# Performance work log

Hardware: AMD Instinct MI355X
Metric: run time of the kernel (lower is better)

## Reference

```python
import jax, jax.numpy as jnp
import numpy as np

B, C, H, W = 8, 256, 128, 128
NH, WS = 8, 8
HD = C // NH
WNH, WNW = H // WS, W // WS


def _rel_pos_index():
    coords = np.stack(np.meshgrid(np.arange(WS), np.arange(WS), indexing='ij'))  # [2,ws,ws]
    flat = coords.reshape(2, -1)
    rel = (flat[:, :, None] - flat[:, None, :]).transpose(1, 2, 0)  # [ws^2,ws^2,2]
    rel[..., 0] += WS - 1
    rel[..., 1] += WS - 1
    rel[..., 0] *= 2 * WS - 1
    return jnp.asarray(rel.sum(-1))  # [ws^2,ws^2]


def grid_sample(img, grid):
    # Bilinear, padding_mode='zeros', align_corners=True. img [N,C,H,W], grid [N,Hg,Wg,2] (x,y in [-1,1])
    N, Ci, Hi, Wi = img.shape
    gx = (grid[..., 0] + 1.0) * 0.5 * (Wi - 1)
    gy = (grid[..., 1] + 1.0) * 0.5 * (Hi - 1)
    x0 = jnp.floor(gx)
    y0 = jnp.floor(gy)
    x0i = x0.astype(jnp.int32)
    y0i = y0.astype(jnp.int32)
    wx1 = gx - x0
    wx0 = 1.0 - wx1
    wy1 = gy - y0
    wy0 = 1.0 - wy1
    nb = jnp.arange(N)[:, None, None]

    def corner(yi, xi, wgt):
        valid = (yi >= 0) & (yi < Hi) & (xi >= 0) & (xi < Wi)
        yc = jnp.clip(yi, 0, Hi - 1)
        xc = jnp.clip(xi, 0, Wi - 1)
        val = img[nb, :, yc, xc]  # [N,Hg,Wg,C]
        return val * (wgt * valid)[..., None]

    out = (corner(y0i, x0i, wy0 * wx0) + corner(y0i, x0i + 1, wy0 * wx1)
           + corner(y0i + 1, x0i, wy1 * wx0) + corner(y0i + 1, x0i + 1, wy1 * wx1))
    return jnp.transpose(out, (0, 3, 1, 2))


def setup_inputs() -> dict:
    key = jax.random.key(0)
    ks = jax.random.split(key, 10)
    f = lambda k, s, sc=1.0: jax.random.normal(k, s, dtype=jnp.float32) * sc
    return {
        'x': f(ks[0], (B, C, H, W)),
        'qkv_w': f(ks[1], (3 * C, C), 0.02),
        'qkv_b': f(ks[2], (3 * C,), 0.02),
        'bias_w': f(ks[3], (2 * NH, C), 0.02),
        'bias_b': f(ks[4], (2 * NH,), 0.02),
        'scale_w': f(ks[5], (2 * NH, C), 0.02),
        'scale_b': f(ks[6], (2 * NH,), 0.02),
        'proj_w': f(ks[7], (C, C), 0.02),
        'proj_b': f(ks[8], (C,), 0.02),
        'rpb_table': f(ks[9], ((2 * WS - 1) ** 2, NH), 0.02),
    }


def reference(x, qkv_w, qkv_b, bias_w, bias_b, scale_w, scale_b, proj_w, proj_b, rpb_table):
    scale = HD ** -0.5
    N = B * NH
    # ---- deterministic base sampling coordinates (shift=0, no padding since H,W % WS == 0) ----
    lin_w = jnp.linspace(-1.0, 1.0, W)
    lin_h = jnp.linspace(-1.0, 1.0, H)
    winref_w = lin_w.reshape(WNW, WS).mean(-1)  # window centers along width
    winref_h = lin_h.reshape(WNH, WS).mean(-1)
    off_w = jnp.arange(WS) * 2.0 / (W - 1)
    off_w = off_w - off_w.mean()
    off_h = jnp.arange(WS) * 2.0 / (H - 1)
    off_h = off_h - off_h.mean()
    base_x = jnp.broadcast_to(winref_w[None, None, :, None] + off_w[None, None, None, :], (WNH, WS, WNW, WS))
    base_y = jnp.broadcast_to((winref_h[:, None] + off_h[None, :])[:, :, None, None], (WNH, WS, WNW, WS))
    # ---- predicted per-head per-window biases & scales ----
    xp = jax.nn.leaky_relu(x.reshape(B, C, WNH, WS, WNW, WS).mean((3, 5)))  # [B,C,WNH,WNW]
    biases = (jnp.einsum('oc,bchw->bohw', bias_w, xp) + bias_b[None, :, None, None]).reshape(N, 2, WNH, WNW)
    bx = biases[:, 0] / WNW  # sampling_biases[:,0] / (w // ws)
    by = biases[:, 1] / WNH
    scales = (jnp.einsum('oc,bchw->bohw', scale_w, xp) + scale_b[None, :, None, None]).reshape(N, 2, WNH, WNW)
    sx, sy = scales[:, 0], scales[:, 1]
    # final = base + local_offsets * scale + bias (broadcast [N,WNH,1,WNW,1] over window interior)
    cx = base_x[None] + off_w[None, None, None, None, :] * sx[:, :, None, :, None] + bx[:, :, None, :, None]
    cy = base_y[None] + off_h[None, None, :, None, None] * sy[:, :, None, :, None] + by[:, :, None, :, None]
    grid = jnp.stack([cx, cy], -1).reshape(N, H, W, 2)
    # ---- qkv via 1x1 conv ----
    qkv = (jnp.einsum('oc,bchw->bohw', qkv_w, x) + qkv_b[None, :, None, None]).reshape(B, 3, NH, HD, H, W)
    q = qkv[:, 0].reshape(N, HD, H, W)
    k = qkv[:, 1].reshape(N, HD, H, W)
    v = qkv[:, 2].reshape(N, HD, H, W)
    ksamp = grid_sample(k, grid)
    vsamp = grid_sample(v, grid)

    def win(t):  # [N,HD,H,W] -> [B, nWin, NH, WS*WS, HD]
        t = t.reshape(B, NH, HD, WNH, WS, WNW, WS)
        return jnp.transpose(t, (0, 3, 5, 1, 4, 6, 2)).reshape(B, WNH * WNW, NH, WS * WS, HD)

    qw, kw, vw = win(q), win(ksamp), win(vsamp)
    rpb = jnp.transpose(rpb_table[_rel_pos_index().reshape(-1)].reshape(WS * WS, WS * WS, NH), (2, 0, 1))
    attn = jnp.einsum('bwhqd,bwhkd->bwhqk', qw, kw) * scale + rpb[None, None]
    attn = jax.nn.softmax(attn, axis=-1)
    out = jnp.einsum('bwhqk,bwhkd->bwhqd', attn, vw)
    out = out.reshape(B, WNH, WNW, NH, WS, WS, HD)
    out = jnp.transpose(out, (0, 3, 6, 1, 4, 2, 5)).reshape(B, C, H, W)
    out = jnp.einsum('oc,bchw->bohw', proj_w, out) + proj_b[None, :, None, None]
    return out
```

## Files before the change

kernel.cpp:

```cpp
#include <hip/hip_runtime.h>
#include <hip/hip_fp16.h>

#define B_ 8
#define C_ 256
#define H_ 128
#define W_ 128
#define NH_ 8
#define WS_ 8
#define HD_ 32
#define WN_ 16
#define NWIN_ 256
#define HW_ 16384

typedef unsigned short ushort_t;
typedef unsigned int uint_t;
typedef __attribute__((ext_vector_type(8))) short short8;
typedef _Float16 __attribute__((ext_vector_type(8))) half8;
typedef __attribute__((ext_vector_type(4))) float f32x4;

__device__ __forceinline__ ushort_t bf16_rtn(float x) {
    uint_t u = __float_as_uint(x);
    return (ushort_t)((u + 0x7FFFu + ((u >> 16) & 1u)) >> 16);
}
__device__ __forceinline__ uint_t bfpack(float a, float b) {
    return (uint_t)bf16_rtn(a) | ((uint_t)bf16_rtn(b) << 16);
}
__device__ __forceinline__ uint_t h2pack(float a, float b) {
    __half2 h = __floats2half2_rn(a, b);
    return __builtin_bit_cast(uint_t, h);
}
__device__ __forceinline__ void gload_lds16(const void* g, void* l) {
    __builtin_amdgcn_global_load_lds(
        (const __attribute__((address_space(1))) unsigned int*)g,
        (__attribute__((address_space(3))) unsigned int*)l,
        16, 0, 0);
}

__global__ __launch_bounds__(256) void wpack_kernel(const float* __restrict__ w,
                            ushort_t* __restrict__ wpk) {
    int u = blockIdx.x*256 + threadIdx.x;
    int lane = u & 63;
    int f    = (u >> 6) & 3;
    int kk   = (u >> 8) & 1;
    int ks   = (u >> 9) & 3;
    int wm   = (u >> 11) & 1;
    int oc   = u >> 12;
    int o = oc*128 + wm*64 + f*16 + (lane & 15);
    int c = ks*64 + kk*32 + (lane >> 4)*8;
    const float* src = w + (size_t)o*256 + c;
    float4 v0 = *(const float4*)src;
    float4 v1 = *(const float4*)(src + 4);
    uint4 Hv;
    Hv.x = bfpack(v0.x, v0.y); Hv.y = bfpack(v0.z, v0.w);
    Hv.z = bfpack(v1.x, v1.y); Hv.w = bfpack(v1.z, v1.w);
    ((uint4*)wpk)[u] = Hv;
}

__global__ __launch_bounds__(256) void wconv_kernel(const float* __restrict__ w,
                            ushort_t* __restrict__ wh, int n4) {
    int i = blockIdx.x*256 + threadIdx.x;
    if (i >= n4) return;
    float4 v = ((const float4*)w)[i];
    ((uint2*)wh)[i] = make_uint2(bfpack(v.x, v.y), bfpack(v.z, v.w));
}

__global__ __launch_bounds__(256) void rpb_expand_kernel(const float* __restrict__ rpb_table,
                            float* __restrict__ rpbT) {
    int nh = blockIdx.x;
    int t = threadIdx.x;
    #pragma unroll
    for (int rr = 0; rr < 16; ++rr) {
        int e = t*16 + rr;
        int kcol = e >> 6, qrow = e & 63;
        int yq = qrow >> 3, xq = qrow & 7, yk = kcol >> 3, xk = kcol & 7;
        int idx = (yq - yk + 7)*15 + (xq - xk + 7);
        rpbT[((size_t)nh*64 + kcol)*64 + qrow] = rpb_table[idx*8 + nh];
    }
}

__global__ __launch_bounds__(256) void transpose_split_kernel(const float* __restrict__ x,
                            ushort_t* __restrict__ th, float* __restrict__ xpart) {
    __shared__ float tile[64][65];
    int b = blockIdx.z;
    int p0 = blockIdx.x * 64, c0 = blockIdx.y * 64;
    const float* xsrc = x + (size_t)b*C_*HW_;
    int t = threadIdx.x;
    #pragma unroll
    for (int r = 0; r < 4; ++r) {
        int task = t + r*256;
        int cl = task >> 4, p4 = (task & 15) * 4;
        float4 v = *(const float4*)(xsrc + (size_t)(c0+cl)*HW_ + p0 + p4);
        tile[cl][p4+0] = v.x; tile[cl][p4+1] = v.y; tile[cl][p4+2] = v.z; tile[cl][p4+3] = v.w;
    }
    __syncthreads();
    {
        int h = blockIdx.x >> 1, wbase = (blockIdx.x & 1) * 8;
        #pragma unroll
        for (int r = 0; r < 2; ++r) {
            int task = t + r*256;
            int cl = task >> 3, wx = task & 7;
            float s = 0.f;
            #pragma unroll
            for (int j = 0; j < 8; ++j) s += tile[cl][wx*8+j];
            xpart[(((size_t)b*256 + c0+cl)*128 + h)*16 + wbase + wx] = s;
        }
    }
    ushort_t* thb = th + (size_t)b*HW_*256;
    #pragma unroll
    for (int r = 0; r < 2; ++r) {
        int task = t + r*256;
        int pl = task >> 3, cb = (task & 7) * 8;
        uint4 Hh;
        Hh.x = bfpack(tile[cb+0][pl], tile[cb+1][pl]);
        Hh.y = bfpack(tile[cb+2][pl], tile[cb+3][pl]);
        Hh.z = bfpack(tile[cb+4][pl], tile[cb+5][pl]);
        Hh.w = bfpack(tile[cb+6][pl], tile[cb+7][pl]);
        *(uint4*)(thb + (size_t)(p0+pl)*256 + c0 + cb) = Hh;
    }
}

__global__ __launch_bounds__(256) void pool2_kernel(const float* __restrict__ xpart, float* __restrict__ xp) {
    int bc = blockIdx.x;
    int t = threadIdx.x;
    int wy = t >> 4, wxg = t & 15;
    const float* src = xpart + (size_t)bc*2048;
    float s = 0.f;
    #pragma unroll
    for (int i = 0; i < 8; ++i) s += src[(wy*8+i)*16 + wxg];
    s *= (1.f/64.f);
    xp[(size_t)bc*256 + t] = s > 0.f ? s : 0.01f*s;
}

__global__ __launch_bounds__(256) void params_kernel(const float* __restrict__ xp,
                              const float* __restrict__ bias_w, const float* __restrict__ bias_b,
                              const float* __restrict__ scale_w, const float* __restrict__ scale_b,
                              float* __restrict__ params) {
    __shared__ float xs[256];
    int blk = blockIdx.x;
    int b = blk >> 8, win = blk & 255;
    int t = threadIdx.x;
    xs[t] = xp[((size_t)(b*256 + t))*256 + win];
    __syncthreads();
    if (t < 32) {
        int which = t >> 4;
        int o = t & 15;
        const float* Wm = which ? scale_w : bias_w;
        float acc = which ? scale_b[o] : bias_b[o];
        for (int c = 0; c < 256; ++c) acc += Wm[o*256 + c] * xs[c];
        int nh = o >> 1, comp = o & 1;
        int n = b*8 + nh;
        float v = which ? acc : 3.96875f * acc;
        params[((size_t)(n*256 + win))*4 + which*2 + comp] = v;
    }
}

__global__ __launch_bounds__(256) void mgemm_qkvt3_kernel(const ushort_t* __restrict__ wpk,
                            const ushort_t* __restrict__ xt,
                            const float* __restrict__ bias,
                            ushort_t* __restrict__ qt, ushort_t* __restrict__ kv) {
    __shared__ __align__(16) uint4 Bbuf[2][1024];
    int bid = blockIdx.x;
    int orig = (bid & 7) * 768 + (bid >> 3);
    int oc = orig % 6;
    int rest = orig / 6;
    int p0 = (rest & 127) * 128;
    int zb = rest >> 7;
    int o0 = oc * 128;
    const ushort_t* xh = xt + (size_t)zb*HW_*256;
    ushort_t* qtb = qt + (size_t)zb*HW_*256;
    ushort_t* kvb = kv + (size_t)zb*8*HW_*64;
    int t = threadIdx.x;
    int lane = t & 63, wid = t >> 6;
    int wm = wid >> 1, wn = wid & 1;
    int qi = lane >> 4, rl = lane & 15;

    const ushort_t* wpkA = wpk + (size_t)(oc*2 + wm)*16384;

    f32x4 acc[4][4];
    #pragma unroll
    for (int f = 0; f < 4; ++f)
        #pragma unroll
        for (int g = 0; g < 4; ++g)
            acc[f][g] = (f32x4){0.f, 0.f, 0.f, 0.f};

    auto STAGE = [&](int ks, int bsel) {
        #pragma unroll
        for (int i = 0; i < 4; ++i) {
            int s = (wid*4 + i)*64 + lane;
            int row = s >> 3;
            int u = (s & 7) ^ (row & 7);
            const ushort_t* g = xh + (size_t)(p0+row)*256 + ks*64 + u*8;
            gload_lds16(g, &Bbuf[bsel][(wid*4 + i)*64]);
        }
    };

    STAGE(0, 0);
    #pragma unroll
    for (int ks = 0; ks < 4; ++ks) {
        int cur = ks & 1;
        if (ks < 3) {
            STAGE(ks+1, cur ^ 1);
            asm volatile("s_waitcnt vmcnt(4)" ::: "memory");
        } else {
            asm volatile("s_waitcnt vmcnt(0)" ::: "memory");
        }
        __builtin_amdgcn_sched_barrier(0);
        __builtin_amdgcn_s_barrier();
        uint4* Bh = Bbuf[cur];
        #pragma unroll
        for (int kk = 0; kk < 2; ++kk) {
            short8 afh[4], bfh[4];
            const ushort_t* wk = wpkA + ((ks*2 + kk)*4)*512 + lane*8;
            #pragma unroll
            for (int f = 0; f < 4; ++f)
                afh[f] = *(const short8*)(wk + f*512);
            #pragma unroll
            for (int g = 0; g < 4; ++g) {
                int row = wn*64 + g*16 + rl;
                int u = (kk*4 + qi) ^ (row & 7);
                bfh[g] = __builtin_bit_cast(short8, Bh[row*8 + u]);
            }
            #pragma unroll
            for (int f = 0; f < 4; ++f)
                #pragma unroll
                for (int g = 0; g < 4; ++g)
                    acc[f][g] = __builtin_amdgcn_mfma_f32_16x16x32_bf16(afh[f], bfh[g], acc[f][g], 0, 0, 0);
        }
        __builtin_amdgcn_s_barrier();
    }

    float* tb = (float*)&Bbuf[0][0];
    #pragma unroll
    for (int pm = 0; pm < 2; ++pm) {
        #pragma unroll
        for (int pn = 0; pn < 2; ++pn) {
            __syncthreads();
            if (wm == pm && wn == pn) {
                #pragma unroll
                for (int f = 0; f < 4; ++f)
                    #pragma unroll
                    for (int g = 0; g < 4; ++g)
                        #pragma unroll
                        for (int r = 0; r < 4; ++r)
                            tb[(f*16 + qi*4 + r)*67 + g*16 + rl] = acc[f][g][r];
            }
            __syncthreads();
            {
                int pxl = t >> 2, cg = t & 3;
                size_t pix = p0 + pn*64 + pxl;
                int obase = o0 + pm*64 + cg*16;
                int type = obase >> 8;
                int oo = obase & 255;
                int head = oo >> 5;
                ushort_t* dst = (type == 0)
                    ? qtb + pix*256 + oo
                    : kvb + ((size_t)head*HW_ + pix)*64 + ((type == 2) ? 32 : 0) + (oo & 31);
                float v[16];
                #pragma unroll
                for (int e = 0; e < 16; ++e) v[e] = tb[(cg*16 + e)*67 + pxl];
                float4 b0 = *(const float4*)&bias[obase];
                float4 b1 = *(const float4*)&bias[obase + 4];
                float4 b2 = *(const float4*)&bias[obase + 8];
                float4 b3 = *(const float4*)&bias[obase + 12];
                uint4 H0, H1;
                H0.x = h2pack(v[0]+b0.x,  v[1]+b0.y);  H0.y = h2pack(v[2]+b0.z,  v[3]+b0.w);
                H0.z = h2pack(v[4]+b1.x,  v[5]+b1.y);  H0.w = h2pack(v[6]+b1.z,  v[7]+b1.w);
                H1.x = h2pack(v[8]+b2.x,  v[9]+b2.y);  H1.y = h2pack(v[10]+b2.z, v[11]+b2.w);
                H1.z = h2pack(v[12]+b3.x, v[13]+b3.y); H1.w = h2pack(v[14]+b3.z, v[15]+b3.w);
                *(uint4*)dst = H0;
                *(uint4*)(dst + 8) = H1;
            }
        }
    }
}

__global__ __launch_bounds__(256) void mgemm_proj_kernel(const ushort_t* __restrict__ wp,
                            const ushort_t* __restrict__ at,
                            const float* __restrict__ bias, float* __restrict__ out) {
    __shared__ __align__(16) uint4 smem[2048];
    uint4* Ah = smem; uint4* Bh = smem + 1024;
    int bid = blockIdx.x;
    int orig = (bid & 7) * 256 + (bid >> 3);
    int o0 = (orig % 2) * 128;
    int rest = orig / 2;
    int p0 = (rest & 127) * 128;
    int zb = rest >> 7;
    const ushort_t* xh = at + (size_t)zb*HW_*256;
    float* outb = out + (size_t)zb*C_*HW_;
    int t = threadIdx.x;
    int lane = t & 63, wid = t >> 6;
    int wm = wid >> 1, wn = wid & 1;
    int q = lane >> 4, rl = lane & 15;

    f32x4 acc[4][4];
    #pragma unroll
    for (int f = 0; f < 4; ++f)
        #pragma unroll
        for (int g = 0; g < 4; ++g)
            acc[f][g] = (f32x4){0.f, 0.f, 0.f, 0.f};

    int srow = t >> 1, shalf = t & 1;
    int sw = srow & 7;

    for (int ks = 0; ks < 4; ++ks) {
        int c0 = ks * 64;
        __syncthreads();
        {
            const uint4* a_h = (const uint4*)(wp + (size_t)(o0+srow)*256 + c0);
            const uint4* b_h = (const uint4*)(xh + (size_t)(p0+srow)*256 + c0);
            #pragma unroll
            for (int jj = 0; jj < 4; ++jj) {
                int u = shalf*4 + jj;
                int d = srow*8 + (u ^ sw);
                Ah[d] = a_h[u]; Bh[d] = b_h[u];
            }
        }
        __syncthreads();
        #pragma unroll
        for (int kk = 0; kk < 2; ++kk) {
            short8 afh[4], bfh[4];
            #pragma unroll
            for (int f = 0; f < 4; ++f) {
                int row = wm*64 + f*16 + rl;
                int u = (kk*4 + q) ^ (row & 7);
                afh[f] = __builtin_bit_cast(short8, Ah[row*8 + u]);
            }
            #pragma unroll
            for (int g = 0; g < 4; ++g) {
                int row = wn*64 + g*16 + rl;
                int u = (kk*4 + q) ^ (row & 7);
                bfh[g] = __builtin_bit_cast(short8, Bh[row*8 + u]);
            }
            #pragma unroll
            for (int f = 0; f < 4; ++f)
                #pragma unroll
                for (int g = 0; g < 4; ++g)
                    acc[f][g] = __builtin_amdgcn_mfma_f32_16x16x32_bf16(afh[f], bfh[g], acc[f][g], 0, 0, 0);
        }
    }
    #pragma unroll
    for (int f = 0; f < 4; ++f) {
        float4 bb = *(const float4*)&bias[o0 + wm*64 + f*16 + q*4];
        float bbv[4] = {bb.x, bb.y, bb.z, bb.w};
        #pragma unroll
        for (int g = 0; g < 4; ++g) {
            int p = p0 + wn*64 + g*16 + rl;
            #pragma unroll
            for (int r = 0; r < 4; ++r) {
                int o = o0 + wm*64 + f*16 + q*4 + r;
                outb[(size_t)o*HW_ + p] = acc[f][g][r] + bbv[r];
            }
        }
    }
}

__global__ __launch_bounds__(256) void attn_kernel(const ushort_t* __restrict__ qt,
                            const ushort_t* __restrict__ kv,
                            const float* __restrict__ params_,
                            const float* __restrict__ rpbT,
                            ushort_t* __restrict__ at) {
    __shared__ __align__(16) ushort_t smem[64*40 + 64*40 + 32*72 + 64*40];
    ushort_t (*Q_lds)[40]   = (ushort_t(*)[40])smem;
    ushort_t (*K_lds)[40]   = (ushort_t(*)[40])(smem + 2560);
    ushort_t (*VT_lds)[72]  = (ushort_t(*)[72])(smem + 5120);
    ushort_t (*P_lds)[72]   = (ushort_t(*)[72])smem;
    ushort_t (*OUT_lds)[40] = (ushort_t(*)[40])(smem + 5120 + 2304);

    int b = blockIdx.y;
    int blk = blockIdx.x;
    int win = blk >> 3, nh = blk & 7;
    int wy = win >> 4, wx = win & 15;
    int t = threadIdx.x;
    int lane = t & 63, wid = t >> 6;

    const float* pp = params_ + ((size_t)((b*8 + nh)*256 + win))*4;
    float ox = pp[0], oy = pp[1], sx = pp[2], sy = pp[3];

    const ushort_t* qtb = qt + (size_t)b*HW_*256;
    const ushort_t* kvb = kv + ((size_t)(b*8 + nh))*HW_*64;
    ushort_t* ath = at + (size_t)b*HW_*256;

    {
        int tok = t >> 2, cg = t & 3;
        int i = tok >> 3, j = tok & 7;
        size_t pix = (size_t)(wy*8 + i)*W_ + wx*8 + j;
        *(uint4*)&Q_lds[tok][cg*8] = *(const uint4*)(qtb + pix*256 + nh*32 + cg*8);
    }
    {
        int tokq = lane >> 3, sub = lane & 7;
        #pragma unroll
        for (int r = 0; r < 2; ++r) {
            int tok = wid*16 + r*8 + tokq;
            int i = tok >> 3, j = tok & 7;
            int h = wy*8 + i, wpx = wx*8 + j;
            float gx = (float)wpx + ((float)j - 3.5f)*sx + ox;
            float gy = (float)h  + ((float)i - 3.5f)*sy + oy;
            float x0f = floorf(gx), y0f = floorf(gy);
            int x0 = (int)x0f, y0 = (int)y0f;
            float wx1 = gx - x0f, wy1 = gy - y0f;
            float wxz = 1.f - wx1, wyz = 1.f - wy1;
            int x1 = x0 + 1, y1 = y0 + 1;
            float m00 = wyz*wxz * ((y0>=0 && y0<H_ && x0>=0 && x0<W_) ? 1.f : 0.f);
            float m01 = wyz*wx1 * ((y0>=0 && y0<H_ && x1>=0 && x1<W_) ? 1.f : 0.f);
            float m10 = wy1*wxz * ((y1>=0 && y1<H_ && x0>=0 && x0<W_) ? 1.f : 0.f);
            float m11 = wy1*wx1 * ((y1>=0 && y1<H_ && x1>=0 && x1<W_) ? 1.f : 0.f);
            int x0c = min(max(x0,0),W_-1), x1c = min(max(x1,0),W_-1);
            int y0c = min(max(y0,0),H_-1), y1c = min(max(y1,0),H_-1);
            size_t p00 = (size_t)y0c*W_ + x0c, p01 = (size_t)y0c*W_ + x1c;
            size_t p10 = (size_t)y1c*W_ + x0c, p11 = (size_t)y1c*W_ + x1c;
            __half2 a0 = __float2half2_rn(0.f), a1 = a0, a2 = a0, a3 = a0;
            #define CORNER(PIX, M) { \
                uint4 u = *(const uint4*)(kvb + (PIX)*64 + sub*8); \
                __half2 wv = __float2half2_rn(M); \
                a0 = __hfma2(__builtin_bit_cast(__half2, u.x), wv, a0); \
                a1 = __hfma2(__builtin_bit_cast(__half2, u.y), wv, a1); \
                a2 = __hfma2(__builtin_bit_cast(__half2, u.z), wv, a2); \
                a3 = __hfma2(__builtin_bit_cast(__half2, u.w), wv, a3); }
            CORNER(p00, m00)
            CORNER(p01, m01)
            CORNER(p10, m10)
            CORNER(p11, m11)
            #undef CORNER
            if (sub < 4) {
                uint4 Kv;
                Kv.x = __builtin_bit_cast(uint_t, a0); Kv.y = __builtin_bit_cast(uint_t, a1);
                Kv.z = __builtin_bit_cast(uint_t, a2); Kv.w = __builtin_bit_cast(uint_t, a3);
                *(uint4*)&K_lds[tok][sub*8] = Kv;
            } else {
                int d0 = (sub - 4)*8;
                VT_lds[d0+0][tok] = __half_as_ushort(__low2half(a0));
                VT_lds[d0+1][tok] = __half_as_ushort(__high2half(a0));
                VT_lds[d0+2][tok] = __half_as_ushort(__low2half(a1));
                VT_lds[d0+3][tok] = __half_as_ushort(__high2half(a1));
                VT_lds[d0+4][tok] = __half_as_ushort(__low2half(a2));
                VT_lds[d0+5][tok] = __half_as_ushort(__high2half(a2));
                VT_lds[d0+6][tok] = __half_as_ushort(__low2half(a3));
                VT_lds[d0+7][tok] = __half_as_ushort(__high2half(a3));
            }
        }
    }
    __syncthreads();

    int q = lane >> 4, rl = lane & 15;
    const float scale = 0.17677669529663687f;

    half8 a_frag = *(const half8*)&Q_lds[wid*16 + rl][q*8];
    half8 b_frag[4];
    #pragma unroll
    for (int g = 0; g < 4; ++g)
        b_frag[g] = *(const half8*)&K_lds[g*16 + rl][q*8];
    __syncthreads();

    f32x4 accS[4];
    #pragma unroll
    for (int g = 0; g < 4; ++g)
        accS[g] = __builtin_amdgcn_mfma_f32_16x16x32_f16(a_frag, b_frag[g], (f32x4){0.f,0.f,0.f,0.f}, 0, 0, 0);

    float Sv[4][4];
    const float* rpbb = rpbT + (size_t)nh*4096;
    int m0 = wid*16 + q*4;
    #pragma unroll
    for (int g = 0; g < 4; ++g) {
        float4 rv = *(const float4*)&rpbb[(g*16 + rl)*64 + m0];
        Sv[g][0] = accS[g][0]*scale + rv.x;
        Sv[g][1] = accS[g][1]*scale + rv.y;
        Sv[g][2] = accS[g][2]*scale + rv.z;
        Sv[g][3] = accS[g][3]*scale + rv.w;
    }
    float inv[4];
    #pragma unroll
    for (int r = 0; r < 4; ++r) {
        float pm = fmaxf(fmaxf(Sv[0][r], Sv[1][r]), fmaxf(Sv[2][r], Sv[3][r]));
        pm = fmaxf(pm, __shfl_xor(pm, 1));
        pm = fmaxf(pm, __shfl_xor(pm, 2));
        pm = fmaxf(pm, __shfl_xor(pm, 4));
        pm = fmaxf(pm, __shfl_xor(pm, 8));
        float s = 0.f;
        #pragma unroll
        for (int g = 0; g < 4; ++g) {
            float e = __expf(Sv[g][r] - pm);
            Sv[g][r] = e;
            s += e;
        }
        s += __shfl_xor(s, 1);
        s += __shfl_xor(s, 2);
        s += __shfl_xor(s, 4);
        s += __shfl_xor(s, 8);
        inv[r] = 1.f / s;
    }
    #pragma unroll
    for (int r = 0; r < 4; ++r) {
        int m = wid*16 + q*4 + r;
        #pragma unroll
        for (int g = 0; g < 4; ++g)
            P_lds[m][g*16 + rl] = __half_as_ushort(__float2half(Sv[g][r]*inv[r]));
    }

    f32x4 accO[2] = {(f32x4){0.f,0.f,0.f,0.f}, (f32x4){0.f,0.f,0.f,0.f}};
    #pragma unroll
    for (int ks = 0; ks < 2; ++ks) {
        half8 p_frag = *(const half8*)&P_lds[wid*16 + rl][ks*32 + q*8];
        #pragma unroll
        for (int g2 = 0; g2 < 2; ++g2) {
            half8 v_frag = *(const half8*)&VT_lds[g2*16 + rl][ks*32 + q*8];
            accO[g2] = __builtin_amdgcn_mfma_f32_16x16x32_f16(p_frag, v_frag, accO[g2], 0, 0, 0);
        }
    }
    #pragma unroll
    for (int r = 0; r < 4; ++r) {
        int m = wid*16 + q*4 + r;
        OUT_lds[m][rl]      = bf16_rtn(accO[0][r]);
        OUT_lds[m][16 + rl] = bf16_rtn(accO[1][r]);
    }
    __syncthreads();
    {
        int tok = t >> 2, cg = t & 3;
        int i2 = tok >> 3, j2 = tok & 7;
        size_t pix = (size_t)(wy*8 + i2)*W_ + wx*8 + j2;
        *(uint4*)(ath + pix*256 + nh*32 + cg*8) = *(const uint4*)&OUT_lds[tok][cg*8];
    }
}

extern "C" void kernel_launch(void* const* d_in, const int* in_sizes, int n_in,
                              void* d_out, int out_size, void* d_ws, size_t ws_size,
                              hipStream_t stream) {
    const float* x       = (const float*)d_in[0];
    const float* qkv_w   = (const float*)d_in[1];
    const float* qkv_b   = (const float*)d_in[2];
    const float* bias_w  = (const float*)d_in[3];
    const float* bias_b  = (const float*)d_in[4];
    const float* scale_w = (const float*)d_in[5];
    const float* scale_b = (const float*)d_in[6];
    const float* proj_w  = (const float*)d_in[7];
    const float* proj_b  = (const float*)d_in[8];
    const float* rpb     = (const float*)d_in[9];
    float* out = (float*)d_out;

    char* ws = (char*)d_ws;
    float*    xp       = (float*)ws;     ws += (size_t)524288*4;
    float*    params   = (float*)ws;     ws += (size_t)65536*4;
    float*    xpart    = (float*)ws;     ws += (size_t)4194304*4;
    float*    rpbT     = (float*)ws;     ws += (size_t)8*4096*4;
    ushort_t* wpk      = (ushort_t*)ws;  ws += (size_t)768*256*2;
    ushort_t* wp       = (ushort_t*)ws;  ws += (size_t)256*256*2;
    ushort_t* xt       = (ushort_t*)ws;  ws += (size_t)B_*HW_*256*2;
    ushort_t* at       = (ushort_t*)ws;  ws += (size_t)B_*HW_*256*2;
    ushort_t* qt       = (ushort_t*)ws;  ws += (size_t)B_*HW_*256*2;
    ushort_t* kv       = (ushort_t*)ws;

    wpack_kernel<<<dim3(96), 256, 0, stream>>>(qkv_w, wpk);
    wconv_kernel<<<dim3(64), 256, 0, stream>>>(proj_w, wp, 256*256/4);
    rpb_expand_kernel<<<dim3(NH_), 256, 0, stream>>>(rpb, rpbT);
    transpose_split_kernel<<<dim3(256, 4, B_), 256, 0, stream>>>(x, xt, xpart);
    pool2_kernel <<<dim3(B_*C_), 256, 0, stream>>>(xpart, xp);
    params_kernel<<<dim3(B_*NWIN_), 256, 0, stream>>>(xp, bias_w, bias_b, scale_w, scale_b, params);
    mgemm_qkvt3_kernel<<<dim3(6144), 256, 0, stream>>>(wpk, xt, qkv_b, qt, kv);
    attn_kernel<<<dim3(NH_*NWIN_, B_), 256, 0, stream>>>(qt, kv, params, rpbT, at);
    mgemm_proj_kernel<<<dim3(2048), 256, 0, stream>>>(wp, at, proj_b, out);
}
```

Baseline: 353.3 us.

## Fuse input transpose and pooling into QKV GEMM reading fp32 x directly

Removes the separate transpose_split kernel and its bf16 transposed copy of x. The QKV GEMM now loads fp32 x tiles into shared memory, computes the window partial sums there (only in the oc==0 blocks), and converts to fp16 on the fly for f16 MFMA; the weights are packed to fp16 to match. This saves one write and one read of a 64 MB intermediate, but each x tile is now reloaded in fp32 by six output-channel blocks. It also drops the async global-to-LDS double buffering, and the strided fp32 LDS reads plus per-fragment packing add latency and VALU work.

```diff
diff --git a/kernel.cpp b/kernel.cpp
--- a/kernel.cpp
+++ b/kernel.cpp
@@ -28,12 +28,6 @@
 __device__ __forceinline__ uint_t h2pack(float a, float b) {
     __half2 h = __floats2half2_rn(a, b);
     return __builtin_bit_cast(uint_t, h);
-}
-__device__ __forceinline__ void gload_lds16(const void* g, void* l) {
-    __builtin_amdgcn_global_load_lds(
-        (const __attribute__((address_space(1))) unsigned int*)g,
-        (__attribute__((address_space(3))) unsigned int*)l,
-        16, 0, 0);
 }
 
 __global__ __launch_bounds__(256) void wpack_kernel(const float* __restrict__ w,
@@ -51,8 +45,8 @@
     float4 v0 = *(const float4*)src;
     float4 v1 = *(const float4*)(src + 4);
     uint4 Hv;
-    Hv.x = bfpack(v0.x, v0.y); Hv.y = bfpack(v0.z, v0.w);
-    Hv.z = bfpack(v1.x, v1.y); Hv.w = bfpack(v1.z, v1.w);
+    Hv.x = h2pack(v0.x, v0.y); Hv.y = h2pack(v0.z, v0.w);
+    Hv.z = h2pack(v1.x, v1.y); Hv.w = h2pack(v1.z, v1.w);
     ((uint4*)wpk)[u] = Hv;
 }
 
@@ -75,47 +69,6 @@
         int yq = qrow >> 3, xq = qrow & 7, yk = kcol >> 3, xk = kcol & 7;
         int idx = (yq - yk + 7)*15 + (xq - xk + 7);
         rpbT[((size_t)nh*64 + kcol)*64 + qrow] = rpb_table[idx*8 + nh];
-    }
-}
-
-__global__ __launch_bounds__(256) void transpose_split_kernel(const float* __restrict__ x,
-                            ushort_t* __restrict__ th, float* __restrict__ xpart) {
-    __shared__ float tile[64][65];
-    int b = blockIdx.z;
-    int p0 = blockIdx.x * 64, c0 = blockIdx.y * 64;
-    const float* xsrc = x + (size_t)b*C_*HW_;
-    int t = threadIdx.x;
-    #pragma unroll
-    for (int r = 0; r < 4; ++r) {
-        int task = t + r*256;
-        int cl = task >> 4, p4 = (task & 15) * 4;
-        float4 v = *(const float4*)(xsrc + (size_t)(c0+cl)*HW_ + p0 + p4);
-        tile[cl][p4+0] = v.x; tile[cl][p4+1] = v.y; tile[cl][p4+2] = v.z; tile[cl][p4+3] = v.w;
-    }
-    __syncthreads();
-    {
-        int h = blockIdx.x >> 1, wbase = (blockIdx.x & 1) * 8;
-        #pragma unroll
-        for (int r = 0; r < 2; ++r) {
-            int task = t + r*256;
-            int cl = task >> 3, wx = task & 7;
-            float s = 0.f;
-            #pragma unroll
-            for (int j = 0; j < 8; ++j) s += tile[cl][wx*8+j];
-            xpart[(((size_t)b*256 + c0+cl)*128 + h)*16 + wbase + wx] = s;
-        }
-    }
-    ushort_t* thb = th + (size_t)b*HW_*256;
-    #pragma unroll
-    for (int r = 0; r < 2; ++r) {
-        int task = t + r*256;
-        int pl = task >> 3, cb = (task & 7) * 8;
-        uint4 Hh;
-        Hh.x = bfpack(tile[cb+0][pl], tile[cb+1][pl]);
-        Hh.y = bfpack(tile[cb+2][pl], tile[cb+3][pl]);
-        Hh.z = bfpack(tile[cb+4][pl], tile[cb+5][pl]);
-        Hh.w = bfpack(tile[cb+6][pl], tile[cb+7][pl]);
-        *(uint4*)(thb + (size_t)(p0+pl)*256 + c0 + cb) = Hh;
     }
 }
 
@@ -154,19 +107,21 @@
     }
 }
 
-__global__ __launch_bounds__(256) void mgemm_qkvt3_kernel(const ushort_t* __restrict__ wpk,
-                            const ushort_t* __restrict__ xt,
+__global__ __launch_bounds__(256) void mgemm_qkvf_kernel(const ushort_t* __restrict__ wpk,
+                            const float* __restrict__ x,
                             const float* __restrict__ bias,
-                            ushort_t* __restrict__ qt, ushort_t* __restrict__ kv) {
-    __shared__ __align__(16) uint4 Bbuf[2][1024];
+                            ushort_t* __restrict__ qt, ushort_t* __restrict__ kv,
+                            float* __restrict__ xpart) {
+    __shared__ __align__(16) float Btile[64*129];
     int bid = blockIdx.x;
     int orig = (bid & 7) * 768 + (bid >> 3);
     int oc = orig % 6;
     int rest = orig / 6;
-    int p0 = (rest & 127) * 128;
+    int hrow = rest & 127;
     int zb = rest >> 7;
+    int p0 = hrow * 128;
     int o0 = oc * 128;
-    const ushort_t* xh = xt + (size_t)zb*HW_*256;
+    const float* xb = x + (size_t)zb*C_*HW_;
     ushort_t* qtb = qt + (size_t)zb*HW_*256;
     ushort_t* kvb = kv + (size_t)zb*8*HW_*64;
     int t = threadIdx.x;
@@ -183,53 +138,56 @@
         for (int g = 0; g < 4; ++g)
             acc[f][g] = (f32x4){0.f, 0.f, 0.f, 0.f};
 
-    auto STAGE = [&](int ks, int bsel) {
-        #pragma unroll
-        for (int i = 0; i < 4; ++i) {
-            int s = (wid*4 + i)*64 + lane;
-            int row = s >> 3;
-            int u = (s & 7) ^ (row & 7);
-            const ushort_t* g = xh + (size_t)(p0+row)*256 + ks*64 + u*8;
-            gload_lds16(g, &Bbuf[bsel][(wid*4 + i)*64]);
-        }
-    };
-
-    STAGE(0, 0);
-    #pragma unroll
     for (int ks = 0; ks < 4; ++ks) {
-        int cur = ks & 1;
-        if (ks < 3) {
-            STAGE(ks+1, cur ^ 1);
-            asm volatile("s_waitcnt vmcnt(4)" ::: "memory");
-        } else {
-            asm volatile("s_waitcnt vmcnt(0)" ::: "memory");
-        }
-        __builtin_amdgcn_sched_barrier(0);
-        __builtin_amdgcn_s_barrier();
-        uint4* Bh = Bbuf[cur];
+        int c0 = ks*64;
+        __syncthreads();
+        #pragma unroll
+        for (int r = 0; r < 8; ++r) {
+            int task = t + r*256;
+            int cl = task >> 5, p4 = (task & 31)*4;
+            float4 v = *(const float4*)(xb + (size_t)(c0+cl)*HW_ + p0 + p4);
+            float* dst = &Btile[cl*129 + p4];
+            dst[0]=v.x; dst[1]=v.y; dst[2]=v.z; dst[3]=v.w;
+        }
+        __syncthreads();
+        if (oc == 0) {
+            #pragma unroll
+            for (int r = 0; r < 4; ++r) {
+                int task = t + r*256;
+                int cl = task >> 4, wxg = task & 15;
+                float s = 0.f;
+                #pragma unroll
+                for (int j = 0; j < 8; ++j) s += Btile[cl*129 + wxg*8 + j];
+                xpart[(((size_t)zb*256 + c0+cl)*128 + hrow)*16 + wxg] = s;
+            }
+        }
         #pragma unroll
         for (int kk = 0; kk < 2; ++kk) {
-            short8 afh[4], bfh[4];
+            half8 afh[4], bfh[4];
             const ushort_t* wk = wpkA + ((ks*2 + kk)*4)*512 + lane*8;
             #pragma unroll
             for (int f = 0; f < 4; ++f)
-                afh[f] = *(const short8*)(wk + f*512);
+                afh[f] = *(const half8*)(wk + f*512);
             #pragma unroll
             for (int g = 0; g < 4; ++g) {
-                int row = wn*64 + g*16 + rl;
-                int u = (kk*4 + qi) ^ (row & 7);
-                bfh[g] = __builtin_bit_cast(short8, Bh[row*8 + u]);
+                int pix = wn*64 + g*16 + rl;
+                const float* col = &Btile[(kk*32 + qi*8)*129 + pix];
+                float f0 = col[0*129], f1 = col[1*129], f2 = col[2*129], f3 = col[3*129];
+                float f4 = col[4*129], f5 = col[5*129], f6 = col[6*129], f7 = col[7*129];
+                uint4 bu;
+                bu.x = h2pack(f0, f1); bu.y = h2pack(f2, f3);
+                bu.z = h2pack(f4, f5); bu.w = h2pack(f6, f7);
+                bfh[g] = __builtin_bit_cast(half8, bu);
             }
             #pragma unroll
             for (int f = 0; f < 4; ++f)
                 #pragma unroll
                 for (int g = 0; g < 4; ++g)
-                    acc[f][g] = __builtin_amdgcn_mfma_f32_16x16x32_bf16(afh[f], bfh[g], acc[f][g], 0, 0, 0);
-        }
-        __builtin_amdgcn_s_barrier();
-    }
-
-    float* tb = (float*)&Bbuf[0][0];
+                    acc[f][g] = __builtin_amdgcn_mfma_f32_16x16x32_f16(afh[f], bfh[g], acc[f][g], 0, 0, 0);
+        }
+    }
+
+    float* tb = Btile;
     #pragma unroll
     for (int pm = 0; pm < 2; ++pm) {
         #pragma unroll
@@ -543,7 +501,6 @@
     float*    rpbT     = (float*)ws;     ws += (size_t)8*4096*4;
     ushort_t* wpk      = (ushort_t*)ws;  ws += (size_t)768*256*2;
     ushort_t* wp       = (ushort_t*)ws;  ws += (size_t)256*256*2;
-    ushort_t* xt       = (ushort_t*)ws;  ws += (size_t)B_*HW_*256*2;
     ushort_t* at       = (ushort_t*)ws;  ws += (size_t)B_*HW_*256*2;
     ushort_t* qt       = (ushort_t*)ws;  ws += (size_t)B_*HW_*256*2;
     ushort_t* kv       = (ushort_t*)ws;
@@ -551,10 +508,9 @@
     wpack_kernel<<<dim3(96), 256, 0, stream>>>(qkv_w, wpk);
     wconv_kernel<<<dim3(64), 256, 0, stream>>>(proj_w, wp, 256*256/4);
     rpb_expand_kernel<<<dim3(NH_), 256, 0, stream>>>(rpb, rpbT);
-    transpose_split_kernel<<<dim3(256, 4, B_), 256, 0, stream>>>(x, xt, xpart);
+    mgemm_qkvf_kernel<<<dim3(6144), 256, 0, stream>>>(wpk, x, qkv_b, qt, kv, xpart);
     pool2_kernel <<<dim3(B_*C_), 256, 0, stream>>>(xpart, xp);
     params_kernel<<<dim3(B_*NWIN_), 256, 0, stream>>>(xp, bias_w, bias_b, scale_w, scale_b, params);
-    mgemm_qkvt3_kernel<<<dim3(6144), 256, 0, stream>>>(wpk, xt, qkv_b, qt, kv);
     attn_kernel<<<dim3(NH_*NWIN_, B_), 256, 0, stream>>>(qt, kv, params, rpbT, at);
     mgemm_proj_kernel<<<dim3(2048), 256, 0, stream>>>(wp, at, proj_b, out);
 }
```

New measurement: 341.0 us. 1.04x faster.
